# Kernel tuning notes

Hardware: AMD Instinct MI355X
Metric: run time of the kernel (lower is better)

## Reference

```python
import jax, jax.numpy as jnp
import numpy as np

N, E = 25000, 400000
F, D, H, C, L = 64, 128, 4, 128, 3  # in_feat, hidden, heads, per-head dim, layers
SCALE = 1.0 / np.sqrt(C)

_PNAMES = [f"{nm}{l}" for l in range(L) for nm in ("Wq", "bq", "Wk", "bk", "Wv", "bv", "Ws", "bs")]


def setup_inputs() -> dict:
    key = jax.random.key(0)
    ks = jax.random.split(key, 64)
    inp = {
        "x": jax.random.normal(ks[0], (N, F), jnp.float32),
        "edge_index": jax.random.randint(ks[1], (2, E), 0, N, jnp.int32),
    }
    i = 2
    for l in range(L):
        fin = F if l == 0 else D
        s = 1.0 / np.sqrt(fin)
        shapes = {"Wq": (fin, H * C), "bq": (H * C,), "Wk": (fin, H * C), "bk": (H * C,),
                  "Wv": (fin, H * C), "bv": (H * C,), "Ws": (fin, D), "bs": (D,)}
        for nm, shp in shapes.items():
            scale = s if nm.startswith("W") else 0.01
            inp[f"{nm}{l}"] = jax.random.normal(ks[i], shp, jnp.float32) * scale
            i += 1
    inp["Wfc"] = jax.random.normal(ks[i], (D, 1), jnp.float32) * (1.0 / np.sqrt(D))
    inp["bfc"] = jnp.zeros((1,), jnp.float32)
    return inp


def _conv(x, src, dst, Wq, bq, Wk, bk, Wv, bv, Ws, bs):
    """PyG TransformerConv, heads=H, concat=False (head-mean), root_weight=True."""
    n = x.shape[0]
    q = (x @ Wq + bq).reshape(n, H, C)
    k = (x @ Wk + bk).reshape(n, H, C)
    v = (x @ Wv + bv).reshape(n, H, C)
    # per-edge attention logits: query at dst, key at src  -> [E, H]
    alpha = jnp.einsum("ehc,ehc->eh", q[dst], k[src]) * SCALE
    # scatter-softmax over incoming edges of each destination node
    m = jax.ops.segment_max(alpha, dst, num_segments=n)        # [N, H]
    e = jnp.exp(alpha - m[dst])                                 # [E, H]
    denom = jax.ops.segment_sum(e, dst, num_segments=n)        # [N, H]
    a = e / (denom[dst] + 1e-16)                                # [E, H]
    out = jax.ops.segment_sum(a[:, :, None] * v[src], dst, num_segments=n)  # [N, H, C]
    return out.mean(axis=1) + x @ Ws + bs                       # concat=False -> mean heads; + skip


def reference(x, edge_index,
              Wq0, bq0, Wk0, bk0, Wv0, bv0, Ws0, bs0,
              Wq1, bq1, Wk1, bk1, Wv1, bv1, Ws1, bs1,
              Wq2, bq2, Wk2, bk2, Wv2, bv2, Ws2, bs2,
              Wfc, bfc):
    src, dst = edge_index[0], edge_index[1]
    h = jax.nn.relu(_conv(x, src, dst, Wq0, bq0, Wk0, bk0, Wv0, bv0, Ws0, bs0))
    h = jax.nn.relu(_conv(h, src, dst, Wq1, bq1, Wk1, bk1, Wv1, bv1, Ws1, bs1))
    h = jax.nn.relu(_conv(h, src, dst, Wq2, bq2, Wk2, bk2, Wv2, bv2, Ws2, bs2))
    g = h.mean(axis=0, keepdims=True)                           # [1, D]
    return jax.nn.sigmoid(g @ Wfc + bfc)                        # [1, 1]
```

## Files before the change

kernel.cpp:

```cpp
#include <hip/hip_runtime.h>
#include <hip/hip_bf16.h>
#include <math.h>

#define NNODES 25000
#define NEDGES 400000
#define FIN0 64
#define DHID 128
#define NHEAD 4
#define CDIM 128
#define HC (NHEAD * CDIM)
#define NOUT 1664
#define SCALE 0.088388347648318447f

typedef __attribute__((ext_vector_type(8))) short short8;
typedef __attribute__((ext_vector_type(4))) float floatx4;
typedef __attribute__((ext_vector_type(2))) float fx2;

typedef __attribute__((address_space(3))) unsigned int lds_u32_t;
typedef __attribute__((address_space(1))) const unsigned int glb_u32_t;

__device__ __forceinline__ void gload_lds16(const void* g, void* l) {
    __builtin_amdgcn_global_load_lds((glb_u32_t*)g, (lds_u32_t*)l, 16, 0, 0);
}

__device__ __forceinline__ short f2bf(float v) {
    unsigned u = __float_as_uint(v);
    u = (u + 0x7fffu + ((u >> 16) & 1u)) >> 16;
    return (short)u;
}
__device__ __forceinline__ float bf2f(short s) {
    return __uint_as_float(((unsigned)(unsigned short)s) << 16);
}
__device__ __forceinline__ unsigned cvt_pk_bf16(float lo, float hi) {
    unsigned r;
    asm("v_cvt_pk_bf16_f32 %0, %1, %2" : "=v"(r) : "v"(lo), "v"(hi));
    return r;
}


__global__ __launch_bounds__(256) void cvt_w_kernel(
    const float* __restrict__ Wq, const float* __restrict__ Wk,
    const float* __restrict__ Wv, const float* __restrict__ Ws,
    const float* __restrict__ bq, const float* __restrict__ bk,
    const float* __restrict__ bv, const float* __restrict__ bs,
    short* __restrict__ WT, float* __restrict__ bc, int fin)
{
    __shared__ float tile[32][33];
    int c0 = blockIdx.x * 32;
    int k0 = blockIdx.y * 32;
    int tx = threadIdx.x & 31, ty = threadIdx.x >> 5;

    const float* W; int ldw, cb;
    if (c0 < 512)       { W = Wq; ldw = 512; cb = c0; }
    else if (c0 < 1024) { W = Wk; ldw = 512; cb = c0 - 512; }
    else if (c0 < 1536) { W = Wv; ldw = 512; cb = c0 - 1024; }
    else                { W = Ws; ldw = 128; cb = c0 - 1536; }

#pragma unroll
    for (int i = 0; i < 4; ++i) {
        int k = k0 + ty + i * 8;
        tile[ty + i * 8][tx] = W[(size_t)k * ldw + cb + tx];
    }
    __syncthreads();
#pragma unroll
    for (int i = 0; i < 4; ++i) {
        int c = c0 + ty + i * 8;
        WT[(size_t)c * fin + k0 + tx] = f2bf(tile[tx][ty + i * 8]);
    }

    if (blockIdx.y == 0 && ty == 0) {
        int c = c0 + tx;
        float b;
        if (c < 512)       b = bq[c];
        else if (c < 1024) b = bk[c - 512];
        else if (c < 1536) b = bv[c - 1024];
        else               b = bs[c - 1536];
        bc[c] = b;
    }
}


__global__ void count_kernel(const int* __restrict__ dst, int* __restrict__ deg, int e) {
    int i = blockIdx.x * blockDim.x + threadIdx.x;
    if (i < e) atomicAdd(&deg[dst[i]], 1);
}

__global__ __launch_bounds__(1024) void scan_kernel(
    const int* __restrict__ deg, int* __restrict__ offs,
    int* __restrict__ cnt, int n, int total) {
    __shared__ int sums[1024];
    int t = threadIdx.x;
    int chunk = (n + 1023) / 1024;
    int b = t * chunk;
    int e = min(b + chunk, n);
    int s = 0;
    for (int i = b; i < e; ++i) s += deg[i];
    sums[t] = s;
    __syncthreads();
    for (int o = 1; o < 1024; o <<= 1) {
        int v = (t >= o) ? sums[t - o] : 0;
        __syncthreads();
        sums[t] += v;
        __syncthreads();
    }
    int run = sums[t] - s;
    for (int i = b; i < e; ++i) {
        offs[i] = run;
        run += deg[i];
        cnt[i] = 0;
    }
    if (t == 0) offs[n] = total;
}

__global__ void scatter_kernel(const int* __restrict__ src, const int* __restrict__ dst,
                               const int* __restrict__ offs, int* __restrict__ cnt,
                               int* __restrict__ csr, int e) {
    int i = blockIdx.x * blockDim.x + threadIdx.x;
    if (i < e) {
        int d = dst[i];
        int pos = offs[d] + atomicAdd(&cnt[d], 1);
        csr[pos] = src[i];
    }
}

template<int FIN, bool CVT>
__global__ __launch_bounds__(256) void gemm_qkvs_mfma(
    const void* __restrict__ Xsrc, int n,
    const short* __restrict__ WT, const float* __restrict__ bc,
    short* __restrict__ Qb, unsigned char* __restrict__ KV,
    short* __restrict__ Sb)
{
    constexpr int CPR16 = FIN / 8;
    constexpr int NK = FIN / 32;
    __shared__ short Xs[64 * FIN];

    int t = threadIdx.x;
    int row0 = blockIdx.x * 64;
    int l = t & 63, w = t >> 6;
    int wcol = blockIdx.y * 256 + w * 64;
    bool active = (wcol < NOUT);
    int lr = l & 15, lk = (l >> 4) * 8;
    int cg = (l >> 4) * 4;

    if (CVT) {
        const float* xf = (const float*)Xsrc;
        for (int s = t; s < 64 * CPR16; s += 256) {
            int r = s / CPR16, c = s % CPR16;
            int cs = c ^ (r & 7);
            int gr = row0 + r;
            short8 v = {};
            if (gr < n) {
                float4 f0 = *(const float4*)&xf[(size_t)gr * FIN + cs * 8];
                float4 f1 = *(const float4*)&xf[(size_t)gr * FIN + cs * 8 + 4];
                v[0] = f2bf(f0.x); v[1] = f2bf(f0.y); v[2] = f2bf(f0.z); v[3] = f2bf(f0.w);
                v[4] = f2bf(f1.x); v[5] = f2bf(f1.y); v[6] = f2bf(f1.z); v[7] = f2bf(f1.w);
            }
            *(short8*)&Xs[s * 8] = v;
        }
    } else {
        const short* xb = (const short*)Xsrc;
#pragma unroll
        for (int it = 0; it < CPR16 / 4; ++it) {
            int seg = it * 4 + w;
            int slot = seg * 64 + l;
            int r = slot / CPR16, c = slot % CPR16;
            int cs = c ^ (r & 7);
            const short* src = xb + (size_t)(row0 + r) * FIN + cs * 8;
            gload_lds16(src, &Xs[seg * 512]);
        }
    }
    __syncthreads();
    if (!active) return;

    float4 bias[4];
#pragma unroll
    for (int ni = 0; ni < 4; ++ni)
        bias[ni] = *(const float4*)&bc[wcol + ni * 16 + cg];

    floatx4 acc[4][4] = {};
#pragma unroll
    for (int ks = 0; ks < NK; ++ks) {
        short8 b[4];
#pragma unroll
        for (int ni = 0; ni < 4; ++ni)
            b[ni] = *(const short8*)&WT[(size_t)(wcol + ni * 16 + lr) * FIN + ks * 32 + lk];
        short8 a[4];
        int q = ks * 4 + (l >> 4);
#pragma unroll
        for (int mi = 0; mi < 4; ++mi) {
            int row = mi * 16 + lr;
            a[mi] = *(const short8*)&Xs[(row * CPR16 + (q ^ (row & 7))) * 8];
        }
#pragma unroll
        for (int mi = 0; mi < 4; ++mi)
#pragma unroll
            for (int ni = 0; ni < 4; ++ni)
                acc[mi][ni] = __builtin_amdgcn_mfma_f32_16x16x32_bf16(
                    b[ni], a[mi], acc[mi][ni], 0, 0, 0);
    }

    int kind = (wcol < 512) ? 0 : (wcol < 1024) ? 1 : (wcol < 1536) ? 2 : 3;
#pragma unroll
    for (int mi = 0; mi < 4; ++mi) {
        int gr = row0 + mi * 16 + lr;
        if (gr >= n) continue;
#pragma unroll
        for (int ni = 0; ni < 4; ++ni) {
            int gc = wcol + ni * 16 + cg;
            float v0 = acc[mi][ni][0] + bias[ni].x;
            float v1 = acc[mi][ni][1] + bias[ni].y;
            float v2 = acc[mi][ni][2] + bias[ni].z;
            float v3 = acc[mi][ni][3] + bias[ni].w;
            if (kind == 0) {
                uint2 p;
                p.x = cvt_pk_bf16(v0, v1);
                p.y = cvt_pk_bf16(v2, v3);
                *(uint2*)&Qb[(size_t)gr * 512 + gc] = p;
            } else if (kind == 1) {
                unsigned r8 = (unsigned)__builtin_amdgcn_cvt_pk_fp8_f32(v0, v1, 0, false);
                r8 = (unsigned)__builtin_amdgcn_cvt_pk_fp8_f32(v2, v3, r8, true);
                *(unsigned*)&KV[(size_t)gr * 1024 + (gc - 512)] = r8;
            } else if (kind == 2) {
                unsigned r8 = (unsigned)__builtin_amdgcn_cvt_pk_fp8_f32(v0, v1, 0, false);
                r8 = (unsigned)__builtin_amdgcn_cvt_pk_fp8_f32(v2, v3, r8, true);
                *(unsigned*)&KV[(size_t)gr * 1024 + 512 + (gc - 1024)] = r8;
            } else {
                uint2 p;
                p.x = cvt_pk_bf16(v0, v1);
                p.y = cvt_pk_bf16(v2, v3);
                *(uint2*)&Sb[(size_t)gr * 128 + (gc - 1536)] = p;
            }
        }
    }
}


__device__ __forceinline__ void unpack8(uint4 r, float* f) {
    f[0] = __uint_as_float(r.x << 16);
    f[1] = __uint_as_float(r.x & 0xffff0000u);
    f[2] = __uint_as_float(r.y << 16);
    f[3] = __uint_as_float(r.y & 0xffff0000u);
    f[4] = __uint_as_float(r.z << 16);
    f[5] = __uint_as_float(r.z & 0xffff0000u);
    f[6] = __uint_as_float(r.w << 16);
    f[7] = __uint_as_float(r.w & 0xffff0000u);
}

__device__ __forceinline__ void decf8(unsigned x, unsigned y, float* f) {
    fx2 a = __builtin_amdgcn_cvt_pk_f32_fp8(x, false);
    fx2 b = __builtin_amdgcn_cvt_pk_f32_fp8(x, true);
    fx2 c = __builtin_amdgcn_cvt_pk_f32_fp8(y, false);
    fx2 d = __builtin_amdgcn_cvt_pk_f32_fp8(y, true);
    f[0] = a[0]; f[1] = a[1]; f[2] = b[0]; f[3] = b[1];
    f[4] = c[0]; f[5] = c[1]; f[6] = d[0]; f[7] = d[1];
}

__device__ __forceinline__ float dotk(const float* q, uint2 kr) {
    float f[8];
    decf8(kr.x, kr.y, f);
    float p = 0.f;
#pragma unroll
    for (int j = 0; j < 8; ++j) p = fmaf(q[j], f[j], p);
    return p;
}

__device__ __forceinline__ void accv(float& d, float* acc, float p, uint2 vr) {
    float vf[8];
    decf8(vr.x, vr.y, vf);
    float w = __expf(p * SCALE);
    d += w;
#pragma unroll
    for (int j = 0; j < 8; ++j) acc[j] = fmaf(w, vf[j], acc[j]);
}

__device__ __forceinline__ float redu16(float p) {
#pragma unroll
    for (int o = 1; o < 16; o <<= 1) p += __shfl_xor(p, o);
    return p;
}

__global__ __launch_bounds__(256) void attn_kernel(
    const short* __restrict__ Qb, const unsigned char* __restrict__ KV,
    const int* __restrict__ offs, const int* __restrict__ csr,
    const short* __restrict__ Sb, short* __restrict__ Xo, int n)
{
    int node = (blockIdx.x * blockDim.x + threadIdx.x) >> 6;
    if (node >= n) return;
    int lane = threadIdx.x & 63;

    float qf[8];
    {
        uint4 qr = *(const uint4*)&Qb[(size_t)node * 512 + lane * 8];
        unpack8(qr, qf);
    }

    int beg = offs[node], end = offs[node + 1];
    float d = 0.f;
    float acc[8] = {};

    int e = beg;
    for (; e + 7 < end; e += 8) {
        uint2 kr[8], vr[8];
#pragma unroll
        for (int j = 0; j < 8; ++j) {
            int s = csr[e + j];
            const unsigned char* b = KV + (size_t)s * 1024 + lane * 8;
            kr[j] = *(const uint2*)b;
            vr[j] = *(const uint2*)(b + 512);
        }
        float p[8];
#pragma unroll
        for (int j = 0; j < 8; ++j) p[j] = dotk(qf, kr[j]);
#pragma unroll
        for (int j = 0; j < 8; ++j) p[j] = redu16(p[j]);
#pragma unroll
        for (int j = 0; j < 8; ++j) accv(d, acc, p[j], vr[j]);
    }
    for (; e + 3 < end; e += 4) {
        uint2 kr[4], vr[4];
#pragma unroll
        for (int j = 0; j < 4; ++j) {
            int s = csr[e + j];
            const unsigned char* b = KV + (size_t)s * 1024 + lane * 8;
            kr[j] = *(const uint2*)b;
            vr[j] = *(const uint2*)(b + 512);
        }
        float p[4];
#pragma unroll
        for (int j = 0; j < 4; ++j) p[j] = dotk(qf, kr[j]);
#pragma unroll
        for (int j = 0; j < 4; ++j) p[j] = redu16(p[j]);
#pragma unroll
        for (int j = 0; j < 4; ++j) accv(d, acc, p[j], vr[j]);
    }
    for (; e < end; ++e) {
        int s = csr[e];
        const unsigned char* b = KV + (size_t)s * 1024 + lane * 8;
        uint2 kr = *(const uint2*)b;
        uint2 vr = *(const uint2*)(b + 512);
        float p = redu16(dotk(qf, kr));
        accv(d, acc, p, vr);
    }

    float inv = (d > 0.f) ? 1.f / d : 0.f;
#pragma unroll
    for (int j = 0; j < 8; ++j) acc[j] *= inv;

#pragma unroll
    for (int j = 0; j < 8; ++j) {
        acc[j] += __shfl_xor(acc[j], 16);
        acc[j] += __shfl_xor(acc[j], 32);
    }

    if (lane < 16) {
        int c0 = lane * 8;
        float sf[8];
        uint4 sr = *(const uint4*)&Sb[(size_t)node * 128 + c0];
        unpack8(sr, sf);
        short8 o;
#pragma unroll
        for (int j = 0; j < 8; ++j)
            o[j] = f2bf(fmaxf(acc[j] * 0.25f + sf[j], 0.f));
        *(short8*)&Xo[(size_t)node * 128 + c0] = o;
    }
}

__global__ void colsum_kernel(const short* __restrict__ X, float* __restrict__ g, int n) {
    int c = threadIdx.x;
    int rpb = (n + gridDim.x - 1) / gridDim.x;
    int r0 = blockIdx.x * rpb;
    int r1 = min(r0 + rpb, n);
    float acc = 0.f;
    for (int r = r0; r < r1; ++r) acc += bf2f(X[r * DHID + c]);
    atomicAdd(&g[c], acc);
}

__global__ void final_kernel(const float* __restrict__ g, const float* __restrict__ Wfc,
                             const float* __restrict__ bfc, float* __restrict__ out, float invn) {
    __shared__ float red[128];
    int t = threadIdx.x;
    red[t] = g[t] * invn * Wfc[t];
    __syncthreads();
    for (int o = 64; o > 0; o >>= 1) {
        if (t < o) red[t] += red[t + o];
        __syncthreads();
    }
    if (t == 0) {
        float z = red[0] + bfc[0];
        out[0] = 1.f / (1.f + expf(-z));
    }
}


extern "C" void kernel_launch(void* const* d_in, const int* in_sizes, int n_in,
                              void* d_out, int out_size, void* d_ws, size_t ws_size,
                              hipStream_t stream) {
    const int N = NNODES, E = NEDGES;
    const float* x = (const float*)d_in[0];
    const int* ei = (const int*)d_in[1];
    const int* src = ei;
    const int* dst = ei + E;
    const float* Wfc = (const float*)d_in[26];
    const float* bfc = (const float*)d_in[27];

    size_t off = 0;
    auto alloc = [&](size_t bytes) -> char* {
        char* p = (char*)d_ws + off;
        off += (bytes + 255) & ~(size_t)255;
        return p;
    };
    int* deg   = (int*)alloc((size_t)N * 4);
    int* cnt   = (int*)alloc((size_t)N * 4);
    int* offs  = (int*)alloc((size_t)(N + 1) * 4);
    int* csr   = (int*)alloc((size_t)E * 4);
    short* Qb  = (short*)alloc((size_t)N * HC * 2);
    unsigned char* KV = (unsigned char*)alloc((size_t)N * 1024);
    short* Sb  = (short*)alloc((size_t)N * DHID * 2);
    short* xb1 = (short*)alloc((size_t)(N + 64) * DHID * 2);
    short* xb2 = (short*)alloc((size_t)(N + 64) * DHID * 2);
    short* WT  = (short*)alloc((size_t)NOUT * DHID * 2);
    float* bc  = (float*)alloc((size_t)NOUT * 4);
    float* g   = (float*)alloc(128 * 4);

    hipMemsetAsync(deg, 0, (size_t)N * 4, stream);
    hipMemsetAsync(g, 0, 128 * 4, stream);

    count_kernel<<<(E + 255) / 256, 256, 0, stream>>>(dst, deg, E);
    scan_kernel<<<1, 1024, 0, stream>>>(deg, offs, cnt, N, E);
    scatter_kernel<<<(E + 255) / 256, 256, 0, stream>>>(src, dst, offs, cnt, csr, E);

    int attn_blocks = (N + 3) / 4;
    int gx = (N + 63) / 64;

    const void* xin = x;
    short* xouts[3] = { xb1, xb2, xb1 };
    for (int l = 0; l < 3; ++l) {
        int fin = (l == 0) ? FIN0 : DHID;
        const float* Wq = (const float*)d_in[2 + l * 8 + 0];
        const float* bq = (const float*)d_in[2 + l * 8 + 1];
        const float* Wk = (const float*)d_in[2 + l * 8 + 2];
        const float* bk = (const float*)d_in[2 + l * 8 + 3];
        const float* Wv = (const float*)d_in[2 + l * 8 + 4];
        const float* bv = (const float*)d_in[2 + l * 8 + 5];
        const float* Wss= (const float*)d_in[2 + l * 8 + 6];
        const float* bs = (const float*)d_in[2 + l * 8 + 7];

        dim3 wgrid(NOUT / 32, fin / 32);
        cvt_w_kernel<<<wgrid, 256, 0, stream>>>(
            Wq, Wk, Wv, Wss, bq, bk, bv, bs, WT, bc, fin);

        dim3 ggrid(gx, 7);
        if (l == 0)
            gemm_qkvs_mfma<64, true><<<ggrid, 256, 0, stream>>>(xin, N, WT, bc, Qb, KV, Sb);
        else
            gemm_qkvs_mfma<128, false><<<ggrid, 256, 0, stream>>>(xin, N, WT, bc, Qb, KV, Sb);
        attn_kernel<<<attn_blocks, 256, 0, stream>>>(Qb, KV, offs, csr, Sb, xouts[l], N);
        xin = xouts[l];
    }

    colsum_kernel<<<256, 128, 0, stream>>>(xb1, g, N);
    final_kernel<<<1, 128, 0, stream>>>(g, Wfc, bfc, (float*)d_out, 1.0f / N);
}
```

Baseline: 546.2 us.

## Store K/V head-major and run attention one head at a time

The QKV GEMM now writes K and V in fp8 into separate head-major arrays instead of one interleaved per-node buffer. The attention kernel loops over heads, so the random neighbour gathers for a head only touch that head's K/V slice and can stay cache-resident. Each wave handles 7 nodes per head, with 16 lanes per edge and 4 edges in parallel. Exp weights go to LDS in a first pass and V is accumulated in a second pass, with a fallback loop for nodes of degree above 64. In exchange it re-reads csr and offs once per head, adds block barriers and makes each wave walk its nodes serially on a fixed 1024-block grid, which may cut parallelism and latency hiding.

Measured after the change: 1.094 ms. 100% more time.

```diff
diff --git a/kernel.cpp b/kernel.cpp
--- a/kernel.cpp
+++ b/kernel.cpp
@@ -11,6 +11,11 @@
 #define HC (NHEAD * CDIM)
 #define NOUT 1664
 #define SCALE 0.088388347648318447f
+
+#define ABLK 1024
+#define WPB 4
+#define MPW 7
+#define MAXT 16
 
 typedef __attribute__((ext_vector_type(8))) short short8;
 typedef __attribute__((ext_vector_type(4))) float floatx4;
@@ -127,8 +132,8 @@
 __global__ __launch_bounds__(256) void gemm_qkvs_mfma(
     const void* __restrict__ Xsrc, int n,
     const short* __restrict__ WT, const float* __restrict__ bc,
-    short* __restrict__ Qb, unsigned char* __restrict__ KV,
-    short* __restrict__ Sb)
+    short* __restrict__ Qb, unsigned char* __restrict__ K8,
+    unsigned char* __restrict__ V8, short* __restrict__ Sb)
 {
     constexpr int CPR16 = FIN / 8;
     constexpr int NK = FIN / 32;
@@ -217,13 +222,15 @@
                 p.y = cvt_pk_bf16(v2, v3);
                 *(uint2*)&Qb[(size_t)gr * 512 + gc] = p;
             } else if (kind == 1) {
+                int c = gc - 512;
                 unsigned r8 = (unsigned)__builtin_amdgcn_cvt_pk_fp8_f32(v0, v1, 0, false);
                 r8 = (unsigned)__builtin_amdgcn_cvt_pk_fp8_f32(v2, v3, r8, true);
-                *(unsigned*)&KV[(size_t)gr * 1024 + (gc - 512)] = r8;
+                *(unsigned*)&K8[(((size_t)(c >> 7)) * NNODES + gr) * 128 + (c & 127)] = r8;
             } else if (kind == 2) {
+                int c = gc - 1024;
                 unsigned r8 = (unsigned)__builtin_amdgcn_cvt_pk_fp8_f32(v0, v1, 0, false);
                 r8 = (unsigned)__builtin_amdgcn_cvt_pk_fp8_f32(v2, v3, r8, true);
-                *(unsigned*)&KV[(size_t)gr * 1024 + 512 + (gc - 1024)] = r8;
+                *(unsigned*)&V8[(((size_t)(c >> 7)) * NNODES + gr) * 128 + (c & 127)] = r8;
             } else {
                 uint2 p;
                 p.x = cvt_pk_bf16(v0, v1);
@@ -264,15 +271,6 @@
     return p;
 }
 
-__device__ __forceinline__ void accv(float& d, float* acc, float p, uint2 vr) {
-    float vf[8];
-    decf8(vr.x, vr.y, vf);
-    float w = __expf(p * SCALE);
-    d += w;
-#pragma unroll
-    for (int j = 0; j < 8; ++j) acc[j] = fmaf(w, vf[j], acc[j]);
-}
-
 __device__ __forceinline__ float redu16(float p) {
 #pragma unroll
     for (int o = 1; o < 16; o <<= 1) p += __shfl_xor(p, o);
@@ -280,88 +278,117 @@
 }
 
 __global__ __launch_bounds__(256) void attn_kernel(
-    const short* __restrict__ Qb, const unsigned char* __restrict__ KV,
-    const int* __restrict__ offs, const int* __restrict__ csr,
-    const short* __restrict__ Sb, short* __restrict__ Xo, int n)
+    const short* __restrict__ Qb, const unsigned char* __restrict__ K8,
+    const unsigned char* __restrict__ V8, const int* __restrict__ offs,
+    const int* __restrict__ csr, const short* __restrict__ Sb,
+    short* __restrict__ Xo, int n)
 {
-    int node = (blockIdx.x * blockDim.x + threadIdx.x) >> 6;
-    if (node >= n) return;
-    int lane = threadIdx.x & 63;
-
-    float qf[8];
-    {
-        uint4 qr = *(const uint4*)&Qb[(size_t)node * 512 + lane * 8];
-        unpack8(qr, qf);
-    }
-
-    int beg = offs[node], end = offs[node + 1];
-    float d = 0.f;
-    float acc[8] = {};
-
-    int e = beg;
-    for (; e + 7 < end; e += 8) {
-        uint2 kr[8], vr[8];
-#pragma unroll
-        for (int j = 0; j < 8; ++j) {
-            int s = csr[e + j];
-            const unsigned char* b = KV + (size_t)s * 1024 + lane * 8;
-            kr[j] = *(const uint2*)b;
-            vr[j] = *(const uint2*)(b + 512);
-        }
-        float p[8];
-#pragma unroll
-        for (int j = 0; j < 8; ++j) p[j] = dotk(qf, kr[j]);
-#pragma unroll
-        for (int j = 0; j < 8; ++j) p[j] = redu16(p[j]);
-#pragma unroll
-        for (int j = 0; j < 8; ++j) accv(d, acc, p[j], vr[j]);
-    }
-    for (; e + 3 < end; e += 4) {
-        uint2 kr[4], vr[4];
-#pragma unroll
-        for (int j = 0; j < 4; ++j) {
-            int s = csr[e + j];
-            const unsigned char* b = KV + (size_t)s * 1024 + lane * 8;
-            kr[j] = *(const uint2*)b;
-            vr[j] = *(const uint2*)(b + 512);
-        }
-        float p[4];
-#pragma unroll
-        for (int j = 0; j < 4; ++j) p[j] = dotk(qf, kr[j]);
-#pragma unroll
-        for (int j = 0; j < 4; ++j) p[j] = redu16(p[j]);
-#pragma unroll
-        for (int j = 0; j < 4; ++j) accv(d, acc, p[j], vr[j]);
-    }
-    for (; e < end; ++e) {
-        int s = csr[e];
-        const unsigned char* b = KV + (size_t)s * 1024 + lane * 8;
-        uint2 kr = *(const uint2*)b;
-        uint2 vr = *(const uint2*)(b + 512);
-        float p = redu16(dotk(qf, kr));
-        accv(d, acc, p, vr);
-    }
-
-    float inv = (d > 0.f) ? 1.f / d : 0.f;
-#pragma unroll
-    for (int j = 0; j < 8; ++j) acc[j] *= inv;
-
-#pragma unroll
-    for (int j = 0; j < 8; ++j) {
-        acc[j] += __shfl_xor(acc[j], 16);
-        acc[j] += __shfl_xor(acc[j], 32);
-    }
-
-    if (lane < 16) {
-        int c0 = lane * 8;
-        float sf[8];
-        uint4 sr = *(const uint4*)&Sb[(size_t)node * 128 + c0];
-        unpack8(sr, sf);
-        short8 o;
-#pragma unroll
-        for (int j = 0; j < 8; ++j)
-            o[j] = f2bf(fmaxf(acc[j] * 0.25f + sf[j], 0.f));
-        *(short8*)&Xo[(size_t)node * 128 + c0] = o;
+    __shared__ float wlds[WPB][MPW][MAXT * 4];
+    __shared__ float om[WPB][MPW][128];
+
+    int t = threadIdx.x;
+    int w = t >> 6, l = t & 63;
+    int g = l >> 4, i = l & 15;
+    int wid = blockIdx.x * WPB + w;
+    int nbase = wid * MPW;
+
+    for (int h = 0; h < NHEAD; ++h) {
+        const unsigned char* Kt = K8 + (size_t)h * n * 128;
+        const unsigned char* Vt = V8 + (size_t)h * n * 128;
+
+        for (int m = 0; m < MPW; ++m) {
+            int node = nbase + m;
+            if (node >= n) break;
+            int beg = offs[node], end = offs[node + 1];
+            float qf[8];
+            {
+                uint4 qr = *(const uint4*)&Qb[(size_t)node * 512 + h * 128 + i * 8];
+                unpack8(qr, qf);
+            }
+            int ntile = min((end - beg + 3) >> 2, MAXT);
+            for (int tt = 0; tt < ntile; ++tt) {
+                int e = beg + tt * 4 + g;
+                int valid = (e < end);
+                int s = valid ? csr[e] : 0;
+                uint2 kr = *(const uint2*)(Kt + (size_t)s * 128 + i * 8);
+                float p = redu16(dotk(qf, kr));
+                float ww = valid ? __expf(p * SCALE) : 0.f;
+                if (i == 0) wlds[w][m][tt * 4 + g] = ww;
+            }
+        }
+        __syncthreads();
+
+        for (int m = 0; m < MPW; ++m) {
+            int node = nbase + m;
+            if (node >= n) break;
+            int beg = offs[node], end = offs[node + 1];
+            float acc[8] = {};
+            float dl = 0.f;
+            int ntile = min((end - beg + 3) >> 2, MAXT);
+            for (int tt = 0; tt < ntile; ++tt) {
+                int e = beg + tt * 4 + g;
+                int valid = (e < end);
+                int s = valid ? csr[e] : 0;
+                float ww = wlds[w][m][tt * 4 + g];
+                uint2 vr = *(const uint2*)(Vt + (size_t)s * 128 + i * 8);
+                float vf[8];
+                decf8(vr.x, vr.y, vf);
+                dl += ww;
+#pragma unroll
+                for (int j = 0; j < 8; ++j) acc[j] = fmaf(ww, vf[j], acc[j]);
+            }
+            if (end - beg > MAXT * 4) {
+                float qf[8];
+                uint4 qr = *(const uint4*)&Qb[(size_t)node * 512 + h * 128 + i * 8];
+                unpack8(qr, qf);
+                for (int e0 = beg + MAXT * 4; e0 < end; e0 += 4) {
+                    int e = e0 + g;
+                    int valid = (e < end);
+                    int s = valid ? csr[e] : 0;
+                    uint2 kr = *(const uint2*)(Kt + (size_t)s * 128 + i * 8);
+                    float p = redu16(dotk(qf, kr));
+                    float ww = valid ? __expf(p * SCALE) : 0.f;
+                    uint2 vr = *(const uint2*)(Vt + (size_t)s * 128 + i * 8);
+                    float vf[8];
+                    decf8(vr.x, vr.y, vf);
+                    dl += ww;
+#pragma unroll
+                    for (int j = 0; j < 8; ++j) acc[j] = fmaf(ww, vf[j], acc[j]);
+                }
+            }
+#pragma unroll
+            for (int j = 0; j < 8; ++j) {
+                acc[j] += __shfl_xor(acc[j], 16);
+                acc[j] += __shfl_xor(acc[j], 32);
+            }
+            dl += __shfl_xor(dl, 16);
+            dl += __shfl_xor(dl, 32);
+            float inv = (dl > 0.f) ? 1.f / dl : 0.f;
+            if (g == 0) {
+#pragma unroll
+                for (int j = 0; j < 8; ++j) {
+                    float v = acc[j] * inv;
+                    if (h == 0) om[w][m][i * 8 + j] = v;
+                    else        om[w][m][i * 8 + j] += v;
+                }
+            }
+        }
+        __syncthreads();
+    }
+
+    for (int m = 0; m < MPW; ++m) {
+        int node = nbase + m;
+        if (node >= n) break;
+        if (g == 0) {
+            float sf[8];
+            uint4 sr = *(const uint4*)&Sb[(size_t)node * 128 + i * 8];
+            unpack8(sr, sf);
+            short8 o;
+#pragma unroll
+            for (int j = 0; j < 8; ++j)
+                o[j] = f2bf(fmaxf(om[w][m][i * 8 + j] * 0.25f + sf[j], 0.f));
+            *(short8*)&Xo[(size_t)node * 128 + i * 8] = o;
+        }
     }
 }
 
@@ -414,7 +441,8 @@
     int* offs  = (int*)alloc((size_t)(N + 1) * 4);
     int* csr   = (int*)alloc((size_t)E * 4);
     short* Qb  = (short*)alloc((size_t)N * HC * 2);
-    unsigned char* KV = (unsigned char*)alloc((size_t)N * 1024);
+    unsigned char* K8 = (unsigned char*)alloc((size_t)N * 512);
+    unsigned char* V8 = (unsigned char*)alloc((size_t)N * 512);
     short* Sb  = (short*)alloc((size_t)N * DHID * 2);
     short* xb1 = (short*)alloc((size_t)(N + 64) * DHID * 2);
     short* xb2 = (short*)alloc((size_t)(N + 64) * DHID * 2);
@@ -429,7 +457,6 @@
     scan_kernel<<<1, 1024, 0, stream>>>(deg, offs, cnt, N, E);
     scatter_kernel<<<(E + 255) / 256, 256, 0, stream>>>(src, dst, offs, cnt, csr, E);
 
-    int attn_blocks = (N + 3) / 4;
     int gx = (N + 63) / 64;
 
     const void* xin = x;
@@ -451,10 +478,10 @@
 
         dim3 ggrid(gx, 7);
         if (l == 0)
-            gemm_qkvs_mfma<64, true><<<ggrid, 256, 0, stream>>>(xin, N, WT, bc, Qb, KV, Sb);
+            gemm_qkvs_mfma<64, true><<<ggrid, 256, 0, stream>>>(xin, N, WT, bc, Qb, K8, V8, Sb);
         else
-            gemm_qkvs_mfma<128, false><<<ggrid, 256, 0, stream>>>(xin, N, WT, bc, Qb, KV, Sb);
-        attn_kernel<<<attn_blocks, 256, 0, stream>>>(Qb, KV, offs, csr, Sb, xouts[l], N);
+            gemm_qkvs_mfma<128, false><<<ggrid, 256, 0, stream>>>(xin, N, WT, bc, Qb, K8, V8, Sb);
+        attn_kernel<<<ABLK, 256, 0, stream>>>(Qb, K8, V8, offs, csr, Sb, xouts[l], N);
         xin = xouts[l];
     }
 
```
